# Performance work log

Hardware: AMD Instinct MI355X
Metric: run time of the kernel (lower is better)

## Reference

```python
import jax, jax.numpy as jnp
import numpy as np

RADIUS = 0.05  # screen-space splat radius (NDC units), from raster_settings


def setup_inputs() -> dict:
    key = jax.random.key(0)
    k1, k2, k3 = jax.random.split(key, 3)
    B, N, C, H = 1, 4096, 8, 128
    # camera-space points: z in [2,4], xy chosen so NDC projection (x/z) covers [-1,1]
    z = jax.random.uniform(k1, (B, N, 1), minval=2.0, maxval=4.0)
    xy = jax.random.uniform(k2, (B, N, 2), minval=-1.0, maxval=1.0) * z
    points = jnp.concatenate([xy, z], axis=-1)  # [B,N,3]
    features = jax.random.normal(k3, (B, N, C), dtype=jnp.float32)
    return {"points": points, "features": features, "image_size": H, "points_per_pixel": 8}


def reference(points, features, image_size, points_per_pixel):
    B, N, _ = points.shape
    H = W = image_size
    K = points_per_pixel
    C = features.shape[-1]
    r2 = RADIUS * RADIUS

    x, y, z = points[..., 0], points[..., 1], points[..., 2]
    # perspective projection to NDC (focal length 1)
    px = x / z  # [B,N]
    py = y / z

    # pixel centers in NDC [-1,1]
    xs = (jnp.arange(W, dtype=jnp.float32) + 0.5) / W * 2.0 - 1.0
    ys = (jnp.arange(H, dtype=jnp.float32) + 0.5) / H * 2.0 - 1.0
    gy, gx = jnp.meshgrid(ys, xs, indexing="ij")
    gx = gx.reshape(-1)  # [P], P = H*W
    gy = gy.reshape(-1)

    # squared screen-space distance pixel<->point: [B, P, N]
    dx = gx[None, :, None] - px[:, None, :]
    dy = gy[None, :, None] - py[:, None, :]
    dist2 = dx * dx + dy * dy

    hit = (dist2 < r2) & (z[:, None, :] > 0.0)
    NEG = jnp.float32(-1e30)
    # K nearest-in-depth points per pixel among hits (top_k of -z)
    keys = jnp.where(hit, -z[:, None, :], NEG)
    negz, idx = jax.lax.top_k(keys, K)  # [B,P,K]
    valid = negz > NEG * 0.5

    d2k = jnp.take_along_axis(dist2, idx, axis=2)           # [B,P,K]
    fk = jax.vmap(lambda f, i: f[i])(features, idx)          # [B,P,K,C]

    # AlphaCompositor: w = 1 - d2/r^2, front-to-back compositing
    alpha = jnp.where(valid, jnp.clip(1.0 - d2k / r2, 0.0, 1.0), 0.0)
    trans = jnp.cumprod(1.0 - alpha, axis=-1)
    T = jnp.concatenate([jnp.ones_like(alpha[..., :1]), trans[..., :-1]], axis=-1)
    w = alpha * T                                            # [B,P,K]

    out = jnp.einsum("bpk,bpkc->bpc", w, fk)
    return out.reshape(B, H, W, C)
```

## Files before the change

kernel.cpp:

```cpp
#include <hip/hip_runtime.h>
#include <math.h>

#define RADIUS 0.05f
#define NSLICE 8
#define SPCAP 1024
#define HCAP  40
#define HSTR  41

__global__ __launch_bounds__(512) void render_tiles(
    const float* __restrict__ points,
    const float* __restrict__ features,
    float* __restrict__ out,
    int N, int H, int W, int tiles_x)
{
    const float r2 = RADIUS * RADIUS;
    const float inv_r2 = 1.0f / r2;

    __shared__ float4 sp[SPCAP];
    __shared__ float  s_hz[64 * HSTR];
    __shared__ float  s_hd[64 * HSTR];
    __shared__ int    s_hi[64 * HSTR];
    __shared__ int    s_pcnt[64];
    __shared__ int    s_cnt;

    if (threadIdx.x == 0) s_cnt = 0;
    if (threadIdx.x < 64) s_pcnt[threadIdx.x] = 0;
    __syncthreads();

    const int tile = blockIdx.x;
    const int tx = tile % tiles_x;
    const int ty = tile / tiles_x;
    const int x0i = tx * 8;
    const int y0i = ty * 8;

    const float sx = 2.0f / (float)W;
    const float sy = 2.0f / (float)H;
    const float bx0 = ((float)x0i + 0.5f) * sx - 1.0f - RADIUS;
    const float bx1 = ((float)(x0i + 7) + 0.5f) * sx - 1.0f + RADIUS;
    const float by0 = ((float)y0i + 0.5f) * sy - 1.0f - RADIUS;
    const float by1 = ((float)(y0i + 7) + 0.5f) * sy - 1.0f + RADIUS;

    for (int i = threadIdx.x; i < N; i += 512) {
        float x = points[3 * i + 0];
        float y = points[3 * i + 1];
        float z = points[3 * i + 2];
        float px = x / z;
        float py = y / z;
        bool keep = (z > 0.0f) & (px >= bx0) & (px <= bx1) & (py >= by0) & (py <= by1);
        if (keep) {
            int pos = atomicAdd(&s_cnt, 1);
            if (pos < SPCAP) sp[pos] = make_float4(px, py, z, __int_as_float(i));
        }
    }
    __syncthreads();
    const int cnt = min(s_cnt, SPCAP);

    const int pxl = threadIdx.x & 63;
    const int slice = threadIdx.x >> 6;
    const int lx = pxl & 7;
    const int ly = pxl >> 3;
    const int ix = x0i + lx;
    const int iy = y0i + ly;
    const float gx = ((float)ix + 0.5f) * sx - 1.0f;
    const float gy = ((float)iy + 0.5f) * sy - 1.0f;

    for (int c = slice; c < cnt; c += NSLICE) {
        float4 q = sp[c];
        float dx = gx - q.x;
        float dy = gy - q.y;
        float d2 = dx * dx + dy * dy;
        if (d2 < r2) {
            int pos = atomicAdd(&s_pcnt[pxl], 1);
            if (pos < HCAP) {
                s_hz[pxl * HSTR + pos] = q.z;
                s_hd[pxl * HSTR + pos] = d2;
                s_hi[pxl * HSTR + pos] = __float_as_int(q.w);
            }
        }
    }
    __syncthreads();

    if (threadIdx.x < 64) {
        const int m = min(s_pcnt[pxl], HCAP);
        float zk[8];
        int sk[8];
#pragma unroll
        for (int k = 0; k < 8; k++) { zk[k] = 3.0e38f; sk[k] = 0; }

        for (int i = 0; i < m; i++) {
            float z = s_hz[pxl * HSTR + i];
            if (z < zk[7]) {
                int s = i;
#pragma unroll
                for (int k = 0; k < 8; k++) {
                    bool lt = z < zk[k];
                    float tz = zk[k];
                    int ts = sk[k];
                    if (lt) { zk[k] = z; sk[k] = s; z = tz; s = ts; }
                }
            }
        }

        float acc0 = 0.f, acc1 = 0.f, acc2 = 0.f, acc3 = 0.f;
        float acc4 = 0.f, acc5 = 0.f, acc6 = 0.f, acc7 = 0.f;
        float T = 1.0f;
#pragma unroll
        for (int k = 0; k < 8; k++) {
            if (zk[k] < 1.0e30f) {
                float d2 = s_hd[pxl * HSTR + sk[k]];
                int   id = s_hi[pxl * HSTR + sk[k]];
                float alpha = 1.0f - d2 * inv_r2;
                alpha = fminf(fmaxf(alpha, 0.0f), 1.0f);
                float w = alpha * T;
                T *= (1.0f - alpha);
                const float4* f = (const float4*)(features + (size_t)id * 8);
                float4 f0 = f[0];
                float4 f1 = f[1];
                acc0 += w * f0.x; acc1 += w * f0.y; acc2 += w * f0.z; acc3 += w * f0.w;
                acc4 += w * f1.x; acc5 += w * f1.y; acc6 += w * f1.z; acc7 += w * f1.w;
            }
        }

        if (ix < W && iy < H) {
            float4* o = (float4*)(out + (size_t)(iy * W + ix) * 8);
            o[0] = make_float4(acc0, acc1, acc2, acc3);
            o[1] = make_float4(acc4, acc5, acc6, acc7);
        }
    }
}

extern "C" void kernel_launch(void* const* d_in, const int* in_sizes, int n_in,
                              void* d_out, int out_size, void* d_ws, size_t ws_size,
                              hipStream_t stream) {
    const float* points = (const float*)d_in[0];
    const float* features = (const float*)d_in[1];
    float* out = (float*)d_out;

    int N = in_sizes[0] / 3;
    int C = in_sizes[1] / N;
    int P = out_size / C;
    int H = (int)(sqrt((double)P) + 0.5);
    int W = H;
    int tiles_x = (W + 7) / 8;
    int tiles_y = (H + 7) / 8;

    render_tiles<<<tiles_x * tiles_y, 512, 0, stream>>>(points, features, out, N, H, W, tiles_x);
}
```

Measured before the change: 72.45 us.

## Bin points into per-tile lists in a separate pass before rendering

Adds a zeroing kernel and a binning kernel that project each point once and append it to the global list of every 8x8 tile its radius overlaps, using atomics and a fixed capacity per tile. The render kernel then loads only its tile's list instead of having every block scan and project all N points. This removes the redundant all-points scan done by each of the 256 blocks, at the cost of two extra launches and global atomics. The capacity of 160 per tile may drop points in dense tiles, and the 1024-byte count region holds only 256 tiles.

```diff
diff --git a/kernel.cpp b/kernel.cpp
--- a/kernel.cpp
+++ b/kernel.cpp
@@ -3,64 +3,85 @@
 
 #define RADIUS 0.05f
 #define NSLICE 8
-#define SPCAP 1024
+#define TCAP  160
 #define HCAP  40
 #define HSTR  41
 
+__global__ __launch_bounds__(256) void zero_counts(int* __restrict__ cnts, int n) {
+    int i = blockIdx.x * 256 + threadIdx.x;
+    if (i < n) cnts[i] = 0;
+}
+
+__global__ __launch_bounds__(256) void bin_points(
+    const float* __restrict__ points, int N, int H, int W,
+    int tiles_x, int tiles_y,
+    int* __restrict__ cnts, float4* __restrict__ lists)
+{
+    int i = blockIdx.x * 256 + threadIdx.x;
+    if (i >= N) return;
+    float x = points[3 * i + 0];
+    float y = points[3 * i + 1];
+    float z = points[3 * i + 2];
+    if (z <= 0.0f) return;
+    float px = x / z;
+    float py = y / z;
+
+    const float invsx = (float)W * 0.5f;
+    const float invsy = (float)H * 0.5f;
+    int ix0 = (int)floorf((px - RADIUS + 1.0f) * invsx - 0.5f);
+    int ix1 = (int)floorf((px + RADIUS + 1.0f) * invsx - 0.5f) + 1;
+    int iy0 = (int)floorf((py - RADIUS + 1.0f) * invsy - 0.5f);
+    int iy1 = (int)floorf((py + RADIUS + 1.0f) * invsy - 0.5f) + 1;
+    ix0 = max(ix0, 0); iy0 = max(iy0, 0);
+    ix1 = min(ix1, W - 1); iy1 = min(iy1, H - 1);
+    if (ix0 > ix1 || iy0 > iy1) return;
+
+    int tx0 = ix0 >> 3, tx1 = ix1 >> 3;
+    int ty0 = iy0 >> 3, ty1 = iy1 >> 3;
+    float4 rec = make_float4(px, py, z, __int_as_float(i));
+    for (int ty = ty0; ty <= ty1; ty++) {
+        for (int tx = tx0; tx <= tx1; tx++) {
+            int t = ty * tiles_x + tx;
+            int pos = atomicAdd(&cnts[t], 1);
+            if (pos < TCAP) lists[(size_t)t * TCAP + pos] = rec;
+        }
+    }
+}
+
 __global__ __launch_bounds__(512) void render_tiles(
-    const float* __restrict__ points,
     const float* __restrict__ features,
     float* __restrict__ out,
-    int N, int H, int W, int tiles_x)
+    int H, int W, int tiles_x,
+    const int* __restrict__ cnts, const float4* __restrict__ lists)
 {
     const float r2 = RADIUS * RADIUS;
     const float inv_r2 = 1.0f / r2;
 
-    __shared__ float4 sp[SPCAP];
+    __shared__ float4 sp[TCAP];
     __shared__ float  s_hz[64 * HSTR];
     __shared__ float  s_hd[64 * HSTR];
     __shared__ int    s_hi[64 * HSTR];
     __shared__ int    s_pcnt[64];
-    __shared__ int    s_cnt;
 
-    if (threadIdx.x == 0) s_cnt = 0;
+    const int tile = blockIdx.x;
+    const int cnt = min(cnts[tile], TCAP);
+
     if (threadIdx.x < 64) s_pcnt[threadIdx.x] = 0;
+    for (int i = threadIdx.x; i < cnt; i += 512)
+        sp[i] = lists[(size_t)tile * TCAP + i];
     __syncthreads();
 
-    const int tile = blockIdx.x;
     const int tx = tile % tiles_x;
     const int ty = tile / tiles_x;
     const int x0i = tx * 8;
     const int y0i = ty * 8;
-
     const float sx = 2.0f / (float)W;
     const float sy = 2.0f / (float)H;
-    const float bx0 = ((float)x0i + 0.5f) * sx - 1.0f - RADIUS;
-    const float bx1 = ((float)(x0i + 7) + 0.5f) * sx - 1.0f + RADIUS;
-    const float by0 = ((float)y0i + 0.5f) * sy - 1.0f - RADIUS;
-    const float by1 = ((float)(y0i + 7) + 0.5f) * sy - 1.0f + RADIUS;
-
-    for (int i = threadIdx.x; i < N; i += 512) {
-        float x = points[3 * i + 0];
-        float y = points[3 * i + 1];
-        float z = points[3 * i + 2];
-        float px = x / z;
-        float py = y / z;
-        bool keep = (z > 0.0f) & (px >= bx0) & (px <= bx1) & (py >= by0) & (py <= by1);
-        if (keep) {
-            int pos = atomicAdd(&s_cnt, 1);
-            if (pos < SPCAP) sp[pos] = make_float4(px, py, z, __int_as_float(i));
-        }
-    }
-    __syncthreads();
-    const int cnt = min(s_cnt, SPCAP);
 
     const int pxl = threadIdx.x & 63;
     const int slice = threadIdx.x >> 6;
-    const int lx = pxl & 7;
-    const int ly = pxl >> 3;
-    const int ix = x0i + lx;
-    const int iy = y0i + ly;
+    const int ix = x0i + (pxl & 7);
+    const int iy = y0i + (pxl >> 3);
     const float gx = ((float)ix + 0.5f) * sx - 1.0f;
     const float gy = ((float)iy + 0.5f) * sy - 1.0f;
 
@@ -143,6 +164,13 @@
     int W = H;
     int tiles_x = (W + 7) / 8;
     int tiles_y = (H + 7) / 8;
+    int n_tiles = tiles_x * tiles_y;
 
-    render_tiles<<<tiles_x * tiles_y, 512, 0, stream>>>(points, features, out, N, H, W, tiles_x);
+    int* cnts = (int*)d_ws;
+    float4* lists = (float4*)((char*)d_ws + 1024);
+
+    zero_counts<<<(n_tiles + 255) / 256, 256, 0, stream>>>(cnts, n_tiles);
+    bin_points<<<(N + 255) / 256, 256, 0, stream>>>(points, N, H, W,
+                                                    tiles_x, tiles_y, cnts, lists);
+    render_tiles<<<n_tiles, 512, 0, stream>>>(features, out, H, W, tiles_x, cnts, lists);
 }
```

Result: slower. 80.53 us (+11.1%).
